# Kernel optimization log

Hardware: AMD Instinct MI355X
Metric: run time of the kernel (lower is better)

Reference implementation:

```python
import jax, jax.numpy as jnp
import numpy as np

VEC_DIM = 3          # Cl(3,0): 3 positive-signature basis vectors
BASIS_DIM = 1 << VEC_DIM  # 8 basis blades
BATCH, IN_F, OUT_F = 512, 512, 512


def cayley_table(n: int = VEC_DIM) -> np.ndarray:
    """Geometric-product tensor G[i, j, k] for Cl(n,0) with blades as bitmasks.
    e_a * e_b = sign(a,b) * e_{a XOR b}; Euclidean metric so e_i^2 = +1.
    Only 2^(2n) of the 2^(3n) entries are nonzero (highly sparse)."""
    dim = 1 << n
    G = np.zeros((dim, dim, dim), dtype=np.float32)
    for a in range(dim):
        for b in range(dim):
            # sign from counting transpositions to bring blade product to canonical order
            swaps, t = 0, a >> 1
            while t:
                swaps += bin(t & b).count("1")
                t >>= 1
            G[a, b, a ^ b] = -1.0 if (swaps & 1) else 1.0
    return G


def setup_inputs() -> dict:
    key = jax.random.key(0)
    kx, kw, kb = jax.random.split(key, 3)
    x = jax.random.normal(kx, (BATCH, IN_F, BASIS_DIM), dtype=jnp.float32)
    W = jax.random.normal(kw, (IN_F, OUT_F, BASIS_DIM), dtype=jnp.float32)
    b = jax.random.normal(kb, (OUT_F, BASIS_DIM), dtype=jnp.float32)
    G = jnp.asarray(cayley_table())  # exact Cl(3,0) geometric-product tensor
    return {"x": x, "W": W, "b": b, "G": G}


def reference(x, W, b, G):
    # out[b,o,k] = sum_{i,j,p} G[i,j,k] * x[b,p,i] * W[p,o,j]  (+ bias)
    out = jnp.einsum("ijk,bpi,poj->bok", G, x, W)
    return out + b
```

## Files before the change

kernel.cpp:

```cpp
#include <hip/hip_runtime.h>
#include <hip/hip_bf16.h>
#include <stdint.h>

typedef __attribute__((ext_vector_type(8))) short short8;
typedef __attribute__((ext_vector_type(4))) float floatx4;

__device__ __forceinline__ unsigned short bfu(float a) {
    return __builtin_bit_cast(unsigned short, __float2bfloat16(a));
}
__device__ __forceinline__ uint32_t pkbf(float a, float b) {
    return (uint32_t)bfu(a) | ((uint32_t)bfu(b) << 16);
}


__global__ __launch_bounds__(256) void pack_all(
    const float* __restrict__ x, const float* __restrict__ W,
    unsigned short* __restrict__ Abuf, unsigned short* __restrict__ BT)
{
    const int t = threadIdx.x;
    if (blockIdx.x < 512) {
        __shared__ unsigned short TX[4][1024];
        const int b = blockIdx.x;
        const float4* src = (const float4*)(x + ((size_t)b * 512 + 2 * t) * 8);
        float4 f[4] = {src[0], src[1], src[2], src[3]};
        #pragma unroll
        for (int pp = 0; pp < 2; ++pp) {
            const float a0 = f[2*pp].x, a1 = f[2*pp].y, a2 = f[2*pp].z, a3 = f[2*pp].w;
            const float a4 = f[2*pp+1].x, a5 = f[2*pp+1].y, a6 = f[2*pp+1].z, a7 = f[2*pp+1].w;
            const int c = 4 * t + 2 * pp;
            TX[0][c] = bfu(a0 + a4); TX[0][c+1] = bfu(a1 - a5);
            TX[1][c] = bfu(a3 + a7); TX[1][c+1] = bfu(a6 - a2);
            TX[2][c] = bfu(a1 + a5); TX[2][c+1] = bfu(a0 - a4);
            TX[3][c] = bfu(a6 + a2); TX[3][c+1] = bfu(a7 - a3);
        }
        __syncthreads();
        const int tr = t >> 6, off = (t & 63) * 16;
        uint4* dst = (uint4*)(Abuf + (size_t)(2*b + (tr >> 1)) * 2048 + (tr & 1) * 1024 + off);
        const uint4* s4 = (const uint4*)&TX[tr][off];
        dst[0] = s4[0]; dst[1] = s4[1];
    } else {
        const int wb = blockIdx.x - 512;
        const int pbase = (wb & 7) * 64;
        const int o0 = (wb >> 3) * 16;
        const int o = o0 + (t & 15);
        const int pc = t >> 4;
        float R[4][2][2], I[4][2][2];
        #pragma unroll
        for (int u = 0; u < 4; ++u) {
            const float4* src = (const float4*)(W + ((size_t)(pbase + pc * 4 + u) * 512 + o) * 8);
            float4 lo = src[0], hi = src[1];
            R[u][0][0] = lo.x + hi.x;  I[u][0][0] = lo.w + hi.w;
            R[u][0][1] = lo.y - hi.y;  I[u][0][1] = hi.z - lo.z;
            R[u][1][0] = lo.y + hi.y;  I[u][1][0] = hi.z + lo.z;
            R[u][1][1] = lo.x - hi.x;  I[u][1][1] = hi.w - lo.w;
        }
        const int kbase = 2 * pbase + pc * 8;
        #pragma unroll
        for (int part = 0; part < 2; ++part)
            #pragma unroll
            for (int pN = 0; pN < 2; ++pN)
                #pragma unroll
                for (int c = 0; c < 2; ++c) {
                    uint4 v; uint32_t* vv = (uint32_t*)&v;
                    #pragma unroll
                    for (int u = 0; u < 4; ++u) {
                        const float v0 = (part == 0) ? (pN ? I[u][0][c] : R[u][0][c])
                                                     : (pN ? R[u][0][c] : -I[u][0][c]);
                        const float v1 = (part == 0) ? (pN ? I[u][1][c] : R[u][1][c])
                                                     : (pN ? R[u][1][c] : -I[u][1][c]);
                        vv[u] = pkbf(v0, v1);
                    }
                    const int n = 4 * o + 2 * pN + c;
                    *(uint4*)&BT[(size_t)n * 2048 + part * 1024 + kbase] = v;
                }
    }
}

#define GLL(src, dstoff) \
    __builtin_amdgcn_global_load_lds((const __attribute__((address_space(1))) uint32_t*)(src), \
        (__attribute__((address_space(3))) uint32_t*)(smem + (dstoff)), 16, 0, 0)

__global__ __launch_bounds__(256, 4) void gemm_split(
    const unsigned short* __restrict__ AB,
    const unsigned short* __restrict__ BB,
    float* __restrict__ partial)
{
    __shared__ __align__(16) unsigned char smem[32768];
    const int t = threadIdx.x, lane = t & 63, wave = t >> 6;
    const int wm = wave & 1, wn = wave >> 1;
    const int l15 = lane & 15, q = lane >> 4;

    const int lin = blockIdx.y * 32 + blockIdx.x;
    const int xcd = lin & 7, s = lin >> 3;
    const int ks = s & 1;
    const int tn = (xcd & 3) * 8 + ((s >> 1) & 7);
    const int tm = (xcd >> 2) * 8 + (s >> 4);
    const int m0 = tm * 64, v0 = tn * 64;
    const int kb0 = ks * 1024;

    const unsigned short* a_srcs[2]; int a_dst[2];
    const unsigned short* b_srcs[2]; int b_dst[2];
    #pragma unroll
    for (int i = 0; i < 2; ++i) {
        const int sid = (wave * 2 + i) * 64 + lane;
        const int row = sid >> 3, sp = sid & 7, ch = sp ^ (row & 7);
        a_srcs[i] = AB + (size_t)(m0 + row) * 2048 + kb0 + ch * 8;
        a_dst[i] = (wave * 2 + i) * 1024;
        b_srcs[i] = BB + (size_t)(v0 + row) * 2048 + kb0 + ch * 8;
        b_dst[i] = 8192 + (wave * 2 + i) * 1024;
    }

    floatx4 acc[2][2] = {};

    #pragma unroll
    for (int i = 0; i < 2; ++i) { GLL(a_srcs[i], a_dst[i]); GLL(b_srcs[i], b_dst[i]); }

    for (int kt = 0; kt < 16; ++kt) {
        __syncthreads();
        const int cur = (kt & 1) * 16384;
        if (kt + 1 < 16) {
            const int nxt = ((kt + 1) & 1) * 16384;
            const int poff = (kt + 1) * 64;
            #pragma unroll
            for (int i = 0; i < 2; ++i) {
                GLL(a_srcs[i] + poff, nxt + a_dst[i]);
                GLL(b_srcs[i] + poff, nxt + b_dst[i]);
            }
        }
        #pragma unroll
        for (int ks2 = 0; ks2 < 2; ++ks2) {
            const int slot = (ks2 * 4 + q) ^ (l15 & 7);
            short8 af[2], bf[2];
            #pragma unroll
            for (int fm = 0; fm < 2; ++fm)
                af[fm] = *(const short8*)&smem[cur + ((wm * 32 + fm * 16 + l15) * 8 + slot) * 16];
            #pragma unroll
            for (int fn = 0; fn < 2; ++fn)
                bf[fn] = *(const short8*)&smem[cur + 8192 + ((wn * 32 + fn * 16 + l15) * 8 + slot) * 16];
            #pragma unroll
            for (int fm = 0; fm < 2; ++fm)
                #pragma unroll
                for (int fn = 0; fn < 2; ++fn)
                    acc[fm][fn] = __builtin_amdgcn_mfma_f32_16x16x32_bf16(
                        af[fm], bf[fn], acc[fm][fn], 0, 0, 0);
        }
    }

    float* pt = partial + ((size_t)((tm * 32 + tn) * 2 + ks)) * 4096;
    #pragma unroll
    for (int fm = 0; fm < 2; ++fm)
        #pragma unroll
        for (int fn = 0; fn < 2; ++fn)
            #pragma unroll
            for (int rr = 0; rr < 4; ++rr)
                pt[(wm * 32 + fm * 16 + q * 4 + rr) * 64 + wn * 32 + fn * 16 + l15]
                    = acc[fm][fn][rr];
}

__global__ __launch_bounds__(256) void reduce_out(
    const float* __restrict__ partial, const float* __restrict__ bias,
    float* __restrict__ out)
{
    const int tile = blockIdx.x;
    const int tm = tile >> 5, tn = tile & 31;
    const float* p0 = partial + (size_t)(tile * 2 + 0) * 4096;
    const float* p1 = partial + (size_t)(tile * 2 + 1) * 4096;
    const int b0 = tm * 32, o0 = tn * 16;
    const int t = threadIdx.x;
    #pragma unroll
    for (int rnd = 0; rnd < 2; ++rnd) {
        const int pi = rnd * 256 + t;
        const int o_l = pi & 15, b_l = pi >> 4;
        const int r0i = (2 * b_l) * 64 + 4 * o_l;
        const float4 q00 = *(const float4*)&p0[r0i];
        const float4 q01 = *(const float4*)&p0[r0i + 64];
        const float4 q10 = *(const float4*)&p1[r0i];
        const float4 q11 = *(const float4*)&p1[r0i + 64];
        const float Cr00 = q00.x + q10.x, Cr01 = q00.y + q10.y;
        const float Ci00 = q00.z + q10.z, Ci01 = q00.w + q10.w;
        const float Cr10 = q01.x + q11.x, Cr11 = q01.y + q11.y;
        const float Ci10 = q01.z + q11.z, Ci11 = q01.w + q11.w;
        const float a0 = 0.5f * (Cr00 + Cr11), a7 = 0.5f * (Ci00 + Ci11);
        const float a4 = 0.5f * (Cr00 - Cr11), a3 = 0.5f * (Ci00 - Ci11);
        const float a1 = 0.5f * (Cr01 + Cr10), a6 = 0.5f * (Ci01 + Ci10);
        const float a2 = 0.5f * (Ci10 - Ci01), a5 = 0.5f * (Cr10 - Cr01);
        const int o = o0 + o_l, b = b0 + b_l;
        const float* bp = bias + o * 8;
        float4 lo = {a0 + bp[0], a1 + bp[1], a2 + bp[2], a3 + bp[3]};
        float4 hi = {a4 + bp[4], a5 + bp[5], a6 + bp[6], a7 + bp[7]};
        float* op = out + ((size_t)b * 512 + o) * 8;
        *(float4*)op = lo;
        *(float4*)(op + 4) = hi;
    }
}

__device__ __align__(16) const uint32_t SGN[4][4] = {
    {0x00000000u, 0x80000000u, 0x80000000u, 0x80008000u},
    {0x80000000u, 0x00000000u, 0x00000000u, 0x00008000u},
    {0x80000000u, 0x80008000u, 0x00000000u, 0x80000000u},
    {0x00000000u, 0x00008000u, 0x80000000u, 0x00000000u},
};
__device__ __forceinline__ uint32_t swap16(uint32_t a) { return (a >> 16) | (a << 16); }
__device__ __forceinline__ uint4 xperm2(uint4 v, int kp) {
    const bool s1 = (kp & 1) != 0;
    uint32_t x1 = s1 ? v.y : v.x, y1 = s1 ? v.x : v.y, z1 = s1 ? v.w : v.z, w1 = s1 ? v.z : v.w;
    const bool s2 = (kp & 2) != 0;
    uint4 r; r.x = s2 ? z1 : x1; r.y = s2 ? w1 : y1; r.z = s2 ? x1 : z1; r.w = s2 ? y1 : w1;
    return r;
}
__global__ __launch_bounds__(512) void gp_linear_legacy(
    const float* __restrict__ xg_raw, const float* __restrict__ wg,
    const float* __restrict__ bias, float* __restrict__ out)
{
    __shared__ __align__(16) unsigned short As[128 * 64];
    __shared__ __align__(16) unsigned short Bs[8 * 64 * 8];
    const int t = threadIdx.x, lane = t & 63, wave = t >> 6;
    const int m0 = blockIdx.y * 128, n0 = blockIdx.x * 64;
    const int ap = t & 7, akp = (t >> 3) & 3, ab = t >> 5, ak0 = akp * 2;
    const uint4 mask = *(const uint4*)SGN[akp];
    const int wm = wave & 3, wnn = wave >> 2, l15 = lane & 15, q = lane >> 4;
    floatx4 acc[2][2] = {};
    const float4* xg = (const float4*)xg_raw;
    const int bg0 = m0 >> 3;
    float4 ax0, ax1, bw0, bw1;
    {
        const size_t aidx = ((size_t)(bg0 + ab) * 512 + ap) * 2;
        ax0 = xg[aidx]; ax1 = xg[aidx + 1];
        const float* gsrc = wg + (((size_t)wave * 512 + n0) << 3) + (lane << 3);
        bw0 = *(const float4*)gsrc; bw1 = *(const float4*)(gsrc + 4);
    }
    for (int kt = 0; kt < 64; ++kt) {
        __syncthreads();
        {
            uint4 v;
            v.x = pkbf(ax0.x, ax0.y); v.y = pkbf(ax0.z, ax0.w);
            v.z = pkbf(ax1.x, ax1.y); v.w = pkbf(ax1.z, ax1.w);
            uint4 pk = xperm2(v, akp), r0, p1, r1;
            r0.x = pk.x ^ mask.x; r0.y = pk.y ^ mask.y; r0.z = pk.z ^ mask.z; r0.w = pk.w ^ mask.w;
            p1.x = swap16(pk.x); p1.y = swap16(pk.y); p1.z = swap16(pk.z); p1.w = swap16(pk.w);
            r1.x = p1.x ^ mask.x; r1.y = p1.y ^ mask.y; r1.z = p1.z ^ mask.z; r1.w = p1.w ^ mask.w;
            const int row0 = ab * 8 + ak0;
            *(uint4*)&As[row0 * 64 + ((ap ^ ak0) << 3)] = r0;
            *(uint4*)&As[(row0 + 1) * 64 + ((ap ^ (ak0 + 1)) << 3)] = r1;
        }
        {
            uint4 b0;
            b0.x = pkbf(bw0.x, bw0.y); b0.y = pkbf(bw0.z, bw0.w);
            b0.z = pkbf(bw1.x, bw1.y); b0.w = pkbf(bw1.z, bw1.w);
            *(uint4*)&Bs[t << 3] = b0;
        }
        __syncthreads();
        if (kt + 1 < 64) {
            const int p0n = (kt + 1) * 8;
            const size_t aidx = ((size_t)(bg0 + ab) * 512 + p0n + ap) * 2;
            ax0 = xg[aidx]; ax1 = xg[aidx + 1];
            const float* gsrc = wg + (((size_t)(p0n + wave) * 512 + n0) << 3) + (lane << 3);
            bw0 = *(const float4*)gsrc; bw1 = *(const float4*)(gsrc + 4);
        }
        #pragma unroll
        for (int ksx = 0; ksx < 2; ++ksx) {
            const int cb = ksx * 4 + q;
            short8 a[2], bfr[2];
            #pragma unroll
            for (int fm = 0; fm < 2; ++fm) {
                const int row = wm * 32 + fm * 16 + l15;
                a[fm] = *(const short8*)&As[row * 64 + ((cb ^ (l15 & 7)) << 3)];
            }
            #pragma unroll
            for (int fn = 0; fn < 2; ++fn) {
                const int nl = wnn * 32 + fn * 16 + l15;
                bfr[fn] = *(const short8*)&Bs[((cb * 64) + nl) << 3];
            }
            #pragma unroll
            for (int fm = 0; fm < 2; ++fm)
                #pragma unroll
                for (int fn = 0; fn < 2; ++fn)
                    acc[fm][fn] = __builtin_amdgcn_mfma_f32_16x16x32_bf16(a[fm], bfr[fn], acc[fm][fn], 0, 0, 0);
        }
    }
    #pragma unroll
    for (int fm = 0; fm < 2; ++fm)
        #pragma unroll
        for (int fn = 0; fn < 2; ++fn) {
            const int n = n0 + wnn * 32 + fn * 16 + l15;
            #pragma unroll
            for (int r = 0; r < 4; ++r) {
                const int m = m0 + wm * 32 + fm * 16 + q * 4 + r;
                const int bi = m >> 3, k = m & 7;
                out[(size_t)bi * 4096 + n * 8 + k] = acc[fm][fn][r] + bias[n * 8 + k];
            }
        }
}

extern "C" void kernel_launch(void* const* d_in, const int* in_sizes, int n_in,
                              void* d_out, int out_size, void* d_ws, size_t ws_size,
                              hipStream_t stream) {
    const float* x  = (const float*)d_in[0];
    const float* W  = (const float*)d_in[1];
    const float* bb = (const float*)d_in[2];
    float* out = (float*)d_out;

    const size_t abytes = (size_t)1024 * 2048 * sizeof(unsigned short);
    const size_t bbytes = (size_t)2048 * 2048 * sizeof(unsigned short);
    const size_t pbytes = (size_t)512 * 2 * 4096 * sizeof(float);
    if (ws_size >= abytes + bbytes + pbytes) {
        unsigned short* Abuf = (unsigned short*)d_ws;
        unsigned short* Bbuf = (unsigned short*)((char*)d_ws + abytes);
        float* part = (float*)((char*)d_ws + abytes + bbytes);
        pack_all<<<768, 256, 0, stream>>>(x, W, Abuf, Bbuf);
        gemm_split<<<dim3(32, 32), 256, 0, stream>>>(Abuf, Bbuf, part);
        reduce_out<<<512, 256, 0, stream>>>(part, bb, out);
    } else {
        gp_linear_legacy<<<dim3(8, 32), dim3(512), 0, stream>>>(x, W, bb, out);
    }
}
```

Baseline: 92.02 us.

## Replace split-K GEMM and reduce kernel with larger-tile GEMM fusing epilogue

Drops the two-way split-K and the separate reduction kernel. Uses 128x128 tiles with 512-thread blocks covering the full K, then stages accumulators through LDS to apply the Clifford recombination and bias directly. This removes the partial-sum write and read traffic and one kernel launch. The cost is only 128 blocks, fewer than the number of CUs, and longer per-block K loops.

```diff
diff --git a/kernel.cpp b/kernel.cpp
--- a/kernel.cpp
+++ b/kernel.cpp
@@ -80,23 +80,22 @@
     __builtin_amdgcn_global_load_lds((const __attribute__((address_space(1))) uint32_t*)(src), \
         (__attribute__((address_space(3))) uint32_t*)(smem + (dstoff)), 16, 0, 0)
 
-__global__ __launch_bounds__(256, 4) void gemm_split(
+__global__ __launch_bounds__(512, 2) void gemm_big(
     const unsigned short* __restrict__ AB,
     const unsigned short* __restrict__ BB,
-    float* __restrict__ partial)
+    const float* __restrict__ bias,
+    float*       __restrict__ out)
 {
-    __shared__ __align__(16) unsigned char smem[32768];
+    __shared__ __align__(16) unsigned char smem[65536];
     const int t = threadIdx.x, lane = t & 63, wave = t >> 6;
-    const int wm = wave & 1, wn = wave >> 1;
+    const int wm = wave & 3, wn = wave >> 2;
     const int l15 = lane & 15, q = lane >> 4;
 
-    const int lin = blockIdx.y * 32 + blockIdx.x;
+    const int lin = blockIdx.y * 16 + blockIdx.x;
     const int xcd = lin & 7, s = lin >> 3;
-    const int ks = s & 1;
-    const int tn = (xcd & 3) * 8 + ((s >> 1) & 7);
-    const int tm = (xcd >> 2) * 8 + (s >> 4);
-    const int m0 = tm * 64, v0 = tn * 64;
-    const int kb0 = ks * 1024;
+    const int tm = (xcd >> 2) * 4 + (s & 3);
+    const int tn = (xcd & 3) * 4 + (s >> 2);
+    const int m0 = tm * 128, v0 = tn * 128;
 
     const unsigned short* a_srcs[2]; int a_dst[2];
     const unsigned short* b_srcs[2]; int b_dst[2];
@@ -104,22 +103,22 @@
     for (int i = 0; i < 2; ++i) {
         const int sid = (wave * 2 + i) * 64 + lane;
         const int row = sid >> 3, sp = sid & 7, ch = sp ^ (row & 7);
-        a_srcs[i] = AB + (size_t)(m0 + row) * 2048 + kb0 + ch * 8;
+        a_srcs[i] = AB + (size_t)(m0 + row) * 2048 + ch * 8;
         a_dst[i] = (wave * 2 + i) * 1024;
-        b_srcs[i] = BB + (size_t)(v0 + row) * 2048 + kb0 + ch * 8;
-        b_dst[i] = 8192 + (wave * 2 + i) * 1024;
-    }
-
-    floatx4 acc[2][2] = {};
+        b_srcs[i] = BB + (size_t)(v0 + row) * 2048 + ch * 8;
+        b_dst[i] = 16384 + (wave * 2 + i) * 1024;
+    }
+
+    floatx4 acc[2][4] = {};
 
     #pragma unroll
     for (int i = 0; i < 2; ++i) { GLL(a_srcs[i], a_dst[i]); GLL(b_srcs[i], b_dst[i]); }
 
-    for (int kt = 0; kt < 16; ++kt) {
-        __syncthreads();
-        const int cur = (kt & 1) * 16384;
-        if (kt + 1 < 16) {
-            const int nxt = ((kt + 1) & 1) * 16384;
+    for (int kt = 0; kt < 32; ++kt) {
+        __syncthreads();
+        const int cur = (kt & 1) * 32768;
+        if (kt + 1 < 32) {
+            const int nxt = ((kt + 1) & 1) * 32768;
             const int poff = (kt + 1) * 64;
             #pragma unroll
             for (int i = 0; i < 2; ++i) {
@@ -130,67 +129,60 @@
         #pragma unroll
         for (int ks2 = 0; ks2 < 2; ++ks2) {
             const int slot = (ks2 * 4 + q) ^ (l15 & 7);
-            short8 af[2], bf[2];
+            short8 af[2], bf[4];
             #pragma unroll
             for (int fm = 0; fm < 2; ++fm)
                 af[fm] = *(const short8*)&smem[cur + ((wm * 32 + fm * 16 + l15) * 8 + slot) * 16];
             #pragma unroll
-            for (int fn = 0; fn < 2; ++fn)
-                bf[fn] = *(const short8*)&smem[cur + 8192 + ((wn * 32 + fn * 16 + l15) * 8 + slot) * 16];
+            for (int fn = 0; fn < 4; ++fn)
+                bf[fn] = *(const short8*)&smem[cur + 16384 + ((wn * 64 + fn * 16 + l15) * 8 + slot) * 16];
             #pragma unroll
             for (int fm = 0; fm < 2; ++fm)
                 #pragma unroll
-                for (int fn = 0; fn < 2; ++fn)
+                for (int fn = 0; fn < 4; ++fn)
                     acc[fm][fn] = __builtin_amdgcn_mfma_f32_16x16x32_bf16(
                         af[fm], bf[fn], acc[fm][fn], 0, 0, 0);
         }
     }
 
-    float* pt = partial + ((size_t)((tm * 32 + tn) * 2 + ks)) * 4096;
+    float* Cf = (float*)smem;
+    const int b0 = m0 >> 1;
+    __syncthreads();
     #pragma unroll
-    for (int fm = 0; fm < 2; ++fm)
-        #pragma unroll
-        for (int fn = 0; fn < 2; ++fn)
-            #pragma unroll
-            for (int rr = 0; rr < 4; ++rr)
-                pt[(wm * 32 + fm * 16 + q * 4 + rr) * 64 + wn * 32 + fn * 16 + l15]
-                    = acc[fm][fn][rr];
-}
-
-__global__ __launch_bounds__(256) void reduce_out(
-    const float* __restrict__ partial, const float* __restrict__ bias,
-    float* __restrict__ out)
-{
-    const int tile = blockIdx.x;
-    const int tm = tile >> 5, tn = tile & 31;
-    const float* p0 = partial + (size_t)(tile * 2 + 0) * 4096;
-    const float* p1 = partial + (size_t)(tile * 2 + 1) * 4096;
-    const int b0 = tm * 32, o0 = tn * 16;
-    const int t = threadIdx.x;
-    #pragma unroll
-    for (int rnd = 0; rnd < 2; ++rnd) {
-        const int pi = rnd * 256 + t;
-        const int o_l = pi & 15, b_l = pi >> 4;
-        const int r0i = (2 * b_l) * 64 + 4 * o_l;
-        const float4 q00 = *(const float4*)&p0[r0i];
-        const float4 q01 = *(const float4*)&p0[r0i + 64];
-        const float4 q10 = *(const float4*)&p1[r0i];
-        const float4 q11 = *(const float4*)&p1[r0i + 64];
-        const float Cr00 = q00.x + q10.x, Cr01 = q00.y + q10.y;
-        const float Ci00 = q00.z + q10.z, Ci01 = q00.w + q10.w;
-        const float Cr10 = q01.x + q11.x, Cr11 = q01.y + q11.y;
-        const float Ci10 = q01.z + q11.z, Ci11 = q01.w + q11.w;
-        const float a0 = 0.5f * (Cr00 + Cr11), a7 = 0.5f * (Ci00 + Ci11);
-        const float a4 = 0.5f * (Cr00 - Cr11), a3 = 0.5f * (Ci00 - Ci11);
-        const float a1 = 0.5f * (Cr01 + Cr10), a6 = 0.5f * (Ci01 + Ci10);
-        const float a2 = 0.5f * (Ci10 - Ci01), a5 = 0.5f * (Cr10 - Cr01);
-        const int o = o0 + o_l, b = b0 + b_l;
-        const float* bp = bias + o * 8;
-        float4 lo = {a0 + bp[0], a1 + bp[1], a2 + bp[2], a3 + bp[3]};
-        float4 hi = {a4 + bp[4], a5 + bp[5], a6 + bp[6], a7 + bp[7]};
-        float* op = out + ((size_t)b * 512 + o) * 8;
-        *(float4*)op = lo;
-        *(float4*)(op + 4) = hi;
+    for (int h = 0; h < 2; ++h) {
+        if (wn == h) {
+            #pragma unroll
+            for (int fm = 0; fm < 2; ++fm)
+                #pragma unroll
+                for (int fn = 0; fn < 4; ++fn)
+                    #pragma unroll
+                    for (int rr = 0; rr < 4; ++rr)
+                        Cf[(wm * 32 + fm * 16 + q * 4 + rr) * 68 + fn * 16 + l15]
+                            = acc[fm][fn][rr];
+        }
+        __syncthreads();
+        #pragma unroll
+        for (int rnd = 0; rnd < 2; ++rnd) {
+            const int pi = rnd * 512 + t;
+            const int o_l = pi & 15, b_l = pi >> 4;
+            const float* r0 = &Cf[(2 * b_l) * 68 + 4 * o_l];
+            const float* r1 = r0 + 68;
+            const float Cr00 = r0[0], Cr01 = r0[1], Ci00 = r0[2], Ci01 = r0[3];
+            const float Cr10 = r1[0], Cr11 = r1[1], Ci10 = r1[2], Ci11 = r1[3];
+            const float a0 = 0.5f * (Cr00 + Cr11), a7 = 0.5f * (Ci00 + Ci11);
+            const float a4 = 0.5f * (Cr00 - Cr11), a3 = 0.5f * (Ci00 - Ci11);
+            const float a1 = 0.5f * (Cr01 + Cr10), a6 = 0.5f * (Ci01 + Ci10);
+            const float a2 = 0.5f * (Ci10 - Ci01), a5 = 0.5f * (Cr10 - Cr01);
+            const int o = tn * 32 + h * 16 + o_l;
+            const int b = b0 + b_l;
+            const float* bp = bias + o * 8;
+            float4 lo = {a0 + bp[0], a1 + bp[1], a2 + bp[2], a3 + bp[3]};
+            float4 hi = {a4 + bp[4], a5 + bp[5], a6 + bp[6], a7 + bp[7]};
+            float* op = out + ((size_t)b * 512 + o) * 8;
+            *(float4*)op = lo;
+            *(float4*)(op + 4) = hi;
+        }
+        __syncthreads();
     }
 }
 
@@ -302,14 +294,11 @@
 
     const size_t abytes = (size_t)1024 * 2048 * sizeof(unsigned short);
     const size_t bbytes = (size_t)2048 * 2048 * sizeof(unsigned short);
-    const size_t pbytes = (size_t)512 * 2 * 4096 * sizeof(float);
-    if (ws_size >= abytes + bbytes + pbytes) {
+    if (ws_size >= abytes + bbytes) {
         unsigned short* Abuf = (unsigned short*)d_ws;
         unsigned short* Bbuf = (unsigned short*)((char*)d_ws + abytes);
-        float* part = (float*)((char*)d_ws + abytes + bbytes);
         pack_all<<<768, 256, 0, stream>>>(x, W, Abuf, Bbuf);
-        gemm_split<<<dim3(32, 32), 256, 0, stream>>>(Abuf, Bbuf, part);
-        reduce_out<<<512, 256, 0, stream>>>(part, bb, out);
+        gemm_big<<<dim3(16, 8), 512, 0, stream>>>(Abuf, Bbuf, bb, out);
     } else {
         gp_linear_legacy<<<dim3(8, 32), dim3(512), 0, stream>>>(x, W, bb, out);
     }
```

Result: slower. 95.91 us (+4.2%).
